# Kernel optimization log

Measured on AMD Instinct MI355X. Metric: run time of the kernel, lower is better.

The kernel has to match this reference:

```python
import jax, jax.numpy as jnp
import numpy as np

N = 100000      # nodes
E = 1600000     # edges (avg degree 16)
D_IN = 128      # in_channels
D_OUT = 64      # out_channels (heads=1)
SCALE_PARAM = 2.0


def setup_inputs() -> dict:
    key = jax.random.key(0)
    ks = jax.random.split(key, 10)
    x = jax.random.normal(ks[0], (N, D_IN), dtype=jnp.float32)
    edge_index = jax.random.randint(ks[1], (2, E), 0, N, dtype=jnp.int64)
    s = 0.05
    Wq = jax.random.normal(ks[2], (D_IN, D_OUT), dtype=jnp.float32) * s
    bq = jax.random.normal(ks[3], (D_OUT,), dtype=jnp.float32) * s
    Wk = jax.random.normal(ks[4], (D_IN, D_OUT), dtype=jnp.float32) * s
    bk = jax.random.normal(ks[5], (D_OUT,), dtype=jnp.float32) * s
    Wv = jax.random.normal(ks[6], (D_IN, D_OUT), dtype=jnp.float32) * s
    bv = jax.random.normal(ks[7], (D_OUT,), dtype=jnp.float32) * s
    Wskip = jax.random.normal(ks[8], (D_IN, D_OUT), dtype=jnp.float32) * s
    bskip = jax.random.normal(ks[9], (D_OUT,), dtype=jnp.float32) * s
    return {"x": x, "edge_index": edge_index, "Wq": Wq, "bq": bq,
            "Wk": Wk, "bk": bk, "Wv": Wv, "bv": bv,
            "Wskip": Wskip, "bskip": bskip}


def reference(x, edge_index, Wq, bq, Wk, bk, Wv, bv, Wskip, bskip):
    # TransformerConvReducrLayer forward (heads=1, no edge_attr, eval mode)
    q = x @ Wq + bq          # [N, C]
    k = x @ Wk + bk          # [N, C]
    v = x @ Wv + bv          # [N, C]
    src = edge_index[0]      # source node j
    dst = edge_index[1]      # target node i
    inv_sqrt_c = np.float32(1.0 / np.sqrt(D_OUT))
    # per-edge attention logits: (query_i * key_j).sum(-1) / sqrt(C)
    alpha = jnp.sum(q[dst] * k[src], axis=-1) * inv_sqrt_c  # [E]
    # custom non-softmax normalization (global mean/std, torch unbiased std)
    alpha = alpha - jnp.mean(alpha)
    alpha = alpha / ((1.0 / np.float32(SCALE_PARAM)) * jnp.std(alpha, ddof=1))
    alpha = jax.nn.sigmoid(alpha)
    # message = value_j * alpha, scatter-add to target nodes
    msg = v[src] * alpha[:, None]                           # [E, C]
    out = jnp.zeros((N, D_OUT), dtype=x.dtype).at[dst].add(msg)
    # root/skip connection (TransformerConv root_weight=True, beta=False)
    out = out + x @ Wskip + bskip
    return out
```

## Files before the change

### kernel.cpp

```cpp
#include <hip/hip_runtime.h>
#include <math.h>

#define D_IN 128
#define D_OUT 64
#define SCALE_PARAM 2.0f
#define NSLOT 64
#define SLOT_STRIDE 16
#define NPB_LOG 9
#define NPB 512
#define MAXBUCK 256
#define MS_NBLK 256

typedef unsigned short ushortt;
typedef __attribute__((ext_vector_type(8))) short bf16x8;
typedef __attribute__((ext_vector_type(4))) float f32x4;

__device__ __forceinline__ ushortt f2bf(float f) {
    union { float f; unsigned u; } cv; cv.f = f;
    unsigned u = cv.u;
    return (ushortt)((u + 0x7FFFu + ((u >> 16) & 1u)) >> 16);
}
__device__ __forceinline__ unsigned cvt_pk_bf16(float a, float b) {
    unsigned r;
    asm("v_cvt_pk_bf16_f32 %0, %1, %2" : "=v"(r) : "v"(a), "v"(b));
    return r;
}
__device__ __forceinline__ float dot2bf(unsigned a, unsigned b, float c) {
    float d;
    asm("v_dot2_f32_bf16 %0, %1, %2, %3" : "=v"(d) : "v"(a), "v"(b), "v"(c));
    return d;
}
__device__ __forceinline__ float bflo(unsigned w) {
    union { unsigned u; float f; } cv; cv.u = w << 16;
    return cv.f;
}
__device__ __forceinline__ float bfhi(unsigned w) {
    union { unsigned u; float f; } cv; cv.u = w & 0xFFFF0000u;
    return cv.f;
}

__global__ __launch_bounds__(256) void prep_w_kernel(
    const float* __restrict__ Wq, const float* __restrict__ Wk,
    const float* __restrict__ Wv, const float* __restrict__ Ws,
    uint4* __restrict__ wfrag)
{
    const int gid = blockIdx.x * 256 + threadIdx.x;
    const int l  = gid & 63;
    const int ci = (gid >> 6) & 3;
    const int ks = (gid >> 8) & 3;
    const int m  = (gid >> 10) & 3;
    const float* Wm = (m == 0) ? Wq : (m == 1) ? Wk : (m == 2) ? Wv : Ws;
    const int cl = l & 15;
    const int kb8 = (l >> 4) * 8;
    unsigned pk[4];
#pragma unroll
    for (int p = 0; p < 4; ++p) {
        float f0 = Wm[(ks * 32 + kb8 + 2 * p)     * D_OUT + ci * 16 + cl];
        float f1 = Wm[(ks * 32 + kb8 + 2 * p + 1) * D_OUT + ci * 16 + cl];
        pk[p] = (unsigned)f2bf(f0) | ((unsigned)f2bf(f1) << 16);
    }
    wfrag[gid] = make_uint4(pk[0], pk[1], pk[2], pk[3]);
}

__global__ __launch_bounds__(256) void fused_gemm_kernel(
    const float* __restrict__ x, const uint4* __restrict__ wfrag,
    const float* __restrict__ bq, const float* __restrict__ bk,
    const float* __restrict__ bv, const float* __restrict__ bs,
    ushortt* __restrict__ q, ushortt* __restrict__ kk, ushortt* __restrict__ v,
    float* __restrict__ skip, int N)
{
    __shared__ __align__(16) ushortt As[64 * 128];
    char* AsB = (char*)As;

    const int t = threadIdx.x;
    const int w = t >> 6;
    const int l = t & 63;
    const int cl = l & 15;
    const int kb8 = (l >> 4) * 8;
    const int rbase = (l >> 4) * 4;
    const int row0 = blockIdx.x * 64;

    const float* bp = (w == 0) ? bq : (w == 1) ? bk : (w == 2) ? bv : bs;

    float4 xv[8];
#pragma unroll
    for (int i = 0; i < 8; ++i) {
        int f = i * 256 + t;
        int r = f >> 5;
        int k4 = f & 31;
        int grow = row0 + r;
        xv[i] = make_float4(0.f, 0.f, 0.f, 0.f);
        if (grow < N)
            xv[i] = *reinterpret_cast<const float4*>(&x[(size_t)grow * D_IN + k4 * 4]);
    }

    union U8 { uint4 u; bf16x8 v; };
    bf16x8 bfr[4][4];
#pragma unroll
    for (int ks = 0; ks < 4; ++ks)
#pragma unroll
        for (int ci = 0; ci < 4; ++ci) {
            U8 tmp; tmp.u = wfrag[((w * 4 + ks) * 4 + ci) * 64 + l];
            bfr[ks][ci] = tmp.v;
        }
    float4 bias4[4];
#pragma unroll
    for (int ci = 0; ci < 4; ++ci)
        bias4[ci] = reinterpret_cast<const float4*>(bp)[ci * 4 + (l >> 4)];

#pragma unroll
    for (int i = 0; i < 8; ++i) {
        int f = i * 256 + t;
        int r = f >> 5;
        int k4 = f & 31;
        uint2 pk;
        pk.x = cvt_pk_bf16(xv[i].x, xv[i].y);
        pk.y = cvt_pk_bf16(xv[i].z, xv[i].w);
        int addr = r * 256 + ((k4 * 8) ^ ((r & 7) << 4));
        *reinterpret_cast<uint2*>(AsB + addr) = pk;
    }
    __syncthreads();

    f32x4 acc[4][4];
#pragma unroll
    for (int ri = 0; ri < 4; ++ri)
#pragma unroll
        for (int ci = 0; ci < 4; ++ci) acc[ri][ci] = (f32x4)(0.f);

#pragma unroll
    for (int ks = 0; ks < 4; ++ks) {
        bf16x8 afr[4];
#pragma unroll
        for (int ri = 0; ri < 4; ++ri) {
            int row = ri * 16 + cl;
            int kby = ks * 64 + kb8 * 2;
            int addr = row * 256 + (kby ^ ((row & 7) << 4));
            afr[ri] = *reinterpret_cast<const bf16x8*>(AsB + addr);
        }
#pragma unroll
        for (int ri = 0; ri < 4; ++ri)
#pragma unroll
            for (int ci = 0; ci < 4; ++ci)
                acc[ri][ci] = __builtin_amdgcn_mfma_f32_16x16x32_bf16(
                    bfr[ks][ci], afr[ri], acc[ri][ci], 0, 0, 0);
    }

    ushortt* qkv = (w == 0) ? q : (w == 1) ? kk : v;
#pragma unroll
    for (int ri = 0; ri < 4; ++ri) {
        int grow = row0 + ri * 16 + cl;
        if (grow >= N) continue;
        if (w == 3) {
#pragma unroll
            for (int ci = 0; ci < 4; ++ci) {
                float4 o;
                o.x = acc[ri][ci][0] + bias4[ci].x;
                o.y = acc[ri][ci][1] + bias4[ci].y;
                o.z = acc[ri][ci][2] + bias4[ci].z;
                o.w = acc[ri][ci][3] + bias4[ci].w;
                *reinterpret_cast<float4*>(&skip[(size_t)grow * D_OUT + ci * 16 + rbase]) = o;
            }
        } else {
#pragma unroll
            for (int ci = 0; ci < 4; ++ci) {
                uint2 pk;
                pk.x = cvt_pk_bf16(acc[ri][ci][0] + bias4[ci].x,
                                   acc[ri][ci][1] + bias4[ci].y);
                pk.y = cvt_pk_bf16(acc[ri][ci][2] + bias4[ci].z,
                                   acc[ri][ci][3] + bias4[ci].w);
                *reinterpret_cast<uint2*>(&qkv[(size_t)grow * D_OUT + ci * 16 + rbase]) = pk;
            }
        }
    }
}

__global__ __launch_bounds__(256) void coarse_hist_kernel(
    const int* __restrict__ dst, int* __restrict__ ccnt, int E)
{
    __shared__ int lc[MAXBUCK];
    const int t = threadIdx.x;
    if (t < MAXBUCK) lc[t] = 0;
    __syncthreads();
    const int stride = gridDim.x * 256 * 4;
    for (int base = (blockIdx.x * 256 + t) * 4; base < E; base += stride) {
        if (base + 3 < E) {
            int4 d = *reinterpret_cast<const int4*>(&dst[base]);
            atomicAdd(&lc[d.x >> NPB_LOG], 1);
            atomicAdd(&lc[d.y >> NPB_LOG], 1);
            atomicAdd(&lc[d.z >> NPB_LOG], 1);
            atomicAdd(&lc[d.w >> NPB_LOG], 1);
        } else {
            for (int i = base; i < E; ++i) atomicAdd(&lc[dst[i] >> NPB_LOG], 1);
        }
    }
    __syncthreads();
    if (t < MAXBUCK && lc[t]) atomicAdd(&ccnt[t], lc[t]);
}

__global__ void coarse_scan_kernel(const int* __restrict__ ccnt,
                                   int* __restrict__ bb, int* __restrict__ tails,
                                   int NBUCK)
{
    if (threadIdx.x == 0) {
        int run = 0;
        for (int b = 0; b < NBUCK; ++b) {
            bb[b] = run;
            tails[b] = run;
            run += ccnt[b];
        }
        bb[NBUCK] = run;
    }
}

__global__ __launch_bounds__(1024) void multisplit_kernel(
    const int* __restrict__ src, const int* __restrict__ dst,
    int* __restrict__ tails, unsigned* __restrict__ ebuf, int E)
{
    __shared__ int cnt[MAXBUCK];
    __shared__ int cur[MAXBUCK];
    __shared__ int base_l[MAXBUCK];
    const int t = threadIdx.x;
    const int blk = blockIdx.x;
    const int e0 = (int)((long long)blk * E / MS_NBLK);
    const int e1 = (int)((long long)(blk + 1) * E / MS_NBLK);
    if (t < MAXBUCK) { cnt[t] = 0; cur[t] = 0; }
    __syncthreads();
    for (int e = e0 + t; e < e1; e += 1024)
        atomicAdd(&cnt[dst[e] >> NPB_LOG], 1);
    __syncthreads();
    if (t < MAXBUCK) {
        int c = cnt[t];
        base_l[t] = c ? atomicAdd(&tails[t], c) : 0;
    }
    __syncthreads();
    for (int e = e0 + t; e < e1; e += 1024) {
        int d = dst[e];
        int b = d >> NPB_LOG;
        int r = atomicAdd(&cur[b], 1);
        ebuf[base_l[b] + r] = ((unsigned)(d & (NPB - 1)) << 17) | (unsigned)src[e];
    }
}

__global__ __launch_bounds__(512) void fine_sort_kernel(
    const unsigned* __restrict__ ebuf, const int* __restrict__ bb,
    int* __restrict__ sorted_src, int* __restrict__ row_start,
    int N, int NBUCK)
{
    __shared__ int cnt[NPB];
    __shared__ int cur[NPB];
    __shared__ int wsum[8];
    const int t = threadIdx.x;
    const int b = blockIdx.x;
    const int nbase = b << NPB_LOG;
    const int seg0 = bb[b], seg1 = bb[b + 1];

    cnt[t] = 0; cur[t] = 0;
    __syncthreads();
    for (int j = seg0 + t; j < seg1; j += 512)
        atomicAdd(&cnt[ebuf[j] >> 17], 1);
    __syncthreads();

    {
        const int lane = t & 63, wid = t >> 6;
        int c = cnt[t];
        int x = c;
#pragma unroll
        for (int off = 1; off < 64; off <<= 1) {
            int n = __shfl_up(x, off, 64);
            if (lane >= off) x += n;
        }
        if (lane == 63) wsum[wid] = x;
        __syncthreads();
        int woff = 0;
        for (int w = 0; w < wid; ++w) woff += wsum[w];
        int excl = x - c + woff;
        cnt[t] = excl;
        int node = nbase + t;
        if (node < N) row_start[node] = seg0 + excl;
    }
    if (b == NBUCK - 1 && t == 0) row_start[N] = seg1;
    __syncthreads();

    for (int j = seg0 + t; j < seg1; j += 512) {
        unsigned u = ebuf[j];
        int dl = u >> 17;
        int r = atomicAdd(&cur[dl], 1);
        sorted_src[seg0 + cnt[dl] + r] = (int)(u & 0x1FFFFu);
    }
}

__global__ __launch_bounds__(256) void node_logit_kernel(
    const ushortt* __restrict__ q, const ushortt* __restrict__ k,
    const int* __restrict__ sorted_src, const int* __restrict__ row_start,
    float* __restrict__ alpha_sorted, float* __restrict__ slots, int N)
{
    const int t = threadIdx.x;
    const int wid = t >> 6, lane = t & 63;
    const int g = lane >> 3;
    const int c8 = lane & 7;
    const int node = blockIdx.x * 4 + wid;
    float lsum = 0.f, lsq = 0.f;
    if (node < N) {
        const uint4 qw = reinterpret_cast<const uint4*>(q + (size_t)node * D_OUT)[c8];
        const int s0 = row_start[node], s1 = row_start[node + 1];
        for (int j0 = s0; j0 < s1; j0 += 32) {
            const int nb = min(s1 - j0, 32);
            int sv = 0;
            if (lane < nb) sv = sorted_src[j0 + lane];
            uint4 kw[4];
#pragma unroll
            for (int it = 0; it < 4; ++it) {
                int sidx = __shfl(sv, it * 8 + g, 64);
                kw[it] = make_uint4(0u, 0u, 0u, 0u);
                if (it * 8 + g < nb)
                    kw[it] = reinterpret_cast<const uint4*>(k + (size_t)sidx * D_OUT)[c8];
            }
#pragma unroll
            for (int it = 0; it < 4; ++it) {
                const bool valid = it * 8 + g < nb;
                float p = dot2bf(qw.x, kw[it].x, 0.f);
                p = dot2bf(qw.y, kw[it].y, p);
                p = dot2bf(qw.z, kw[it].z, p);
                p = dot2bf(qw.w, kw[it].w, p);
                p += __shfl_xor(p, 1, 8);
                p += __shfl_xor(p, 2, 8);
                p += __shfl_xor(p, 4, 8);
                if (valid && c8 == 0) {
                    float a = p * 0.125f;
                    alpha_sorted[j0 + it * 8 + g] = a;
                    lsum += a;
                    lsq += a * a;
                }
            }
        }
    }
#pragma unroll
    for (int off = 1; off < 64; off <<= 1) {
        lsum += __shfl_xor(lsum, off, 64);
        lsq  += __shfl_xor(lsq,  off, 64);
    }
    __shared__ float red[2][4];
    if (lane == 0) { red[0][wid] = lsum; red[1][wid] = lsq; }
    __syncthreads();
    if (t == 0) {
        float* sl = slots + (blockIdx.x & (NSLOT - 1)) * SLOT_STRIDE;
        atomicAdd(&sl[0], red[0][0] + red[0][1] + red[0][2] + red[0][3]);
        atomicAdd(&sl[1], red[1][0] + red[1][1] + red[1][2] + red[1][3]);
    }
}

__global__ void finalize_stats_kernel(const float* __restrict__ slots,
                                      float* stats, int E) {
    const int lane = threadIdx.x & 63;
    float s  = slots[lane * SLOT_STRIDE];
    float s2 = slots[lane * SLOT_STRIDE + 1];
#pragma unroll
    for (int off = 1; off < 64; off <<= 1) {
        s  += __shfl_xor(s,  off, 64);
        s2 += __shfl_xor(s2, off, 64);
    }
    if (lane == 0) {
        float mean = s / (float)E;
        float var = (s2 - (float)E * mean * mean) / (float)(E - 1);
        stats[2] = mean;
        stats[3] = SCALE_PARAM / sqrtf(var);
    }
}

__global__ __launch_bounds__(256) void node_gather_kernel(
    const ushortt* __restrict__ v, const int* __restrict__ sorted_src,
    const float* __restrict__ alpha_sorted, const int* __restrict__ row_start,
    const float* __restrict__ stats, float* __restrict__ out, int N)
{
    const int t = threadIdx.x;
    const int wid = t >> 6, lane = t & 63;
    const int g = lane >> 3, c8 = lane & 7;
    const int node = blockIdx.x * 4 + wid;
    if (node >= N) return;
    const float mean = stats[2], coef = stats[3];
    float a0 = 0, a1 = 0, a2 = 0, a3 = 0, a4 = 0, a5 = 0, a6 = 0, a7 = 0;
    const int s0 = row_start[node], s1 = row_start[node + 1];
    for (int j0 = s0; j0 < s1; j0 += 32) {
        const int nb = min(s1 - j0, 32);
        int sv = 0;
        float av = 0.f;
        if (lane < nb) {
            sv = sorted_src[j0 + lane];
            float al = alpha_sorted[j0 + lane];
            al = (al - mean) * coef;
            av = 1.f / (1.f + __expf(-al));
        }
        uint4 vw[4];
        float alv[4];
#pragma unroll
        for (int it = 0; it < 4; ++it) {
            int sidx = __shfl(sv, it * 8 + g, 64);
            alv[it] = __shfl(av, it * 8 + g, 64);
            vw[it] = make_uint4(0u, 0u, 0u, 0u);
            if (it * 8 + g < nb)
                vw[it] = reinterpret_cast<const uint4*>(v + (size_t)sidx * D_OUT)[c8];
        }
#pragma unroll
        for (int it = 0; it < 4; ++it) {
            const float al = (it * 8 + g < nb) ? alv[it] : 0.f;
            a0 = fmaf(bflo(vw[it].x), al, a0); a1 = fmaf(bfhi(vw[it].x), al, a1);
            a2 = fmaf(bflo(vw[it].y), al, a2); a3 = fmaf(bfhi(vw[it].y), al, a3);
            a4 = fmaf(bflo(vw[it].z), al, a4); a5 = fmaf(bfhi(vw[it].z), al, a5);
            a6 = fmaf(bflo(vw[it].w), al, a6); a7 = fmaf(bfhi(vw[it].w), al, a7);
        }
    }
#pragma unroll
    for (int off = 8; off < 64; off <<= 1) {
        a0 += __shfl_xor(a0, off, 64); a1 += __shfl_xor(a1, off, 64);
        a2 += __shfl_xor(a2, off, 64); a3 += __shfl_xor(a3, off, 64);
        a4 += __shfl_xor(a4, off, 64); a5 += __shfl_xor(a5, off, 64);
        a6 += __shfl_xor(a6, off, 64); a7 += __shfl_xor(a7, off, 64);
    }
    if (g == 0) {
        float* op = out + (size_t)node * D_OUT + c8 * 8;
        float4 c0 = *reinterpret_cast<float4*>(op);
        float4 c1 = *reinterpret_cast<float4*>(op + 4);
        c0.x += a0; c0.y += a1; c0.z += a2; c0.w += a3;
        c1.x += a4; c1.y += a5; c1.z += a6; c1.w += a7;
        *reinterpret_cast<float4*>(op)     = c0;
        *reinterpret_cast<float4*>(op + 4) = c1;
    }
}

extern "C" void kernel_launch(void* const* d_in, const int* in_sizes, int n_in,
                              void* d_out, int out_size, void* d_ws, size_t ws_size,
                              hipStream_t stream) {
    const float* x     = (const float*)d_in[0];
    const int*   eidx  = (const int*)d_in[1];
    const float* Wq    = (const float*)d_in[2];
    const float* bq    = (const float*)d_in[3];
    const float* Wk    = (const float*)d_in[4];
    const float* bk    = (const float*)d_in[5];
    const float* Wv    = (const float*)d_in[6];
    const float* bv    = (const float*)d_in[7];
    const float* Ws    = (const float*)d_in[8];
    const float* bs    = (const float*)d_in[9];
    float* out = (float*)d_out;

    const int N = in_sizes[0] / D_IN;
    const int E = in_sizes[1] / 2;
    const int* src = eidx;
    const int* dst = eidx + E;
    const int NBUCK = (N + NPB - 1) >> NPB_LOG;

    char* base = (char*)d_ws;
    size_t cur = 0;
    auto carve = [&](size_t bytes) -> char* {
        char* p = base + cur;
        cur = (cur + bytes + 255) & ~(size_t)255;
        return p;
    };
    const size_t nodebf = (size_t)N * D_OUT * sizeof(ushortt);
    ushortt* q          = (ushortt*)carve(nodebf);
    ushortt* k          = (ushortt*)carve(nodebf);
    ushortt* v          = (ushortt*)carve(nodebf);
    float* alpha_sorted = (float*)carve((size_t)E * sizeof(float));
    int*   sorted_src   = (int*)carve((size_t)E * sizeof(int));
    unsigned* ebuf      = (unsigned*)carve((size_t)E * sizeof(unsigned));
    uint4* wfrag        = (uint4*)carve(4096 * sizeof(uint4));
    const size_t ccnt_b  = (MAXBUCK * sizeof(int) + 255) & ~(size_t)255;
    const size_t slots_b = (size_t)NSLOT * SLOT_STRIDE * sizeof(float);
    char*  zreg         = carve(ccnt_b + slots_b + 256);
    int*   ccnt         = (int*)zreg;
    float* slots        = (float*)(zreg + ccnt_b);
    float* stats        = (float*)(zreg + ccnt_b + slots_b);
    int*   row_start    = (int*)carve((size_t)(N + 1) * sizeof(int));
    int*   bb           = (int*)carve((size_t)(MAXBUCK + 1) * sizeof(int));
    int*   tails        = (int*)carve((size_t)MAXBUCK * sizeof(int));

    hipMemsetAsync(zreg, 0, ccnt_b + slots_b + 256, stream);

    prep_w_kernel<<<16, 256, 0, stream>>>(Wq, Wk, Wv, Ws, wfrag);

    coarse_hist_kernel<<<512, 256, 0, stream>>>(dst, ccnt, E);
    coarse_scan_kernel<<<1, 64, 0, stream>>>(ccnt, bb, tails, NBUCK);
    multisplit_kernel<<<MS_NBLK, 1024, 0, stream>>>(src, dst, tails, ebuf, E);

    const int gemm_grid = (N + 63) / 64;
    fused_gemm_kernel<<<gemm_grid, 256, 0, stream>>>(
        x, wfrag, bq, bk, bv, bs, q, k, v, out, N);

    fine_sort_kernel<<<NBUCK, 512, 0, stream>>>(
        ebuf, bb, sorted_src, row_start, N, NBUCK);

    node_logit_kernel<<<(N + 3) / 4, 256, 0, stream>>>(
        q, k, sorted_src, row_start, alpha_sorted, slots, N);
    finalize_stats_kernel<<<1, 64, 0, stream>>>(slots, stats, E);
    node_gather_kernel<<<(N + 3) / 4, 256, 0, stream>>>(
        v, sorted_src, alpha_sorted, row_start, stats, out, N);
}
```

Before: 176.8 us.

## Fuse weight prep with histogram and multisplit with GEMM via block-range dispatch

Merges the weight-fragment prep kernel with the coarse destination histogram into one launch. The multisplit (edge bucketing) kernel is merged into the node GEMM kernel, with the first 512 blocks doing multisplit at 256 threads and the rest doing GEMM rows. The aim is to cut launch count and let the memory-bound edge scatter overlap with the GEMM instead of running serially. Multisplit now uses smaller blocks, twice as many of them, and shared memory reused from the GEMM tile buffer. This may change the per-block atomic contention on the global tails.

```diff
diff --git a/kernel.cpp b/kernel.cpp
--- a/kernel.cpp
+++ b/kernel.cpp
@@ -9,7 +9,8 @@
 #define NPB_LOG 9
 #define NPB 512
 #define MAXBUCK 256
-#define MS_NBLK 256
+#define MSF_NBLK 512
+#define PREP_BLKS 16
 
 typedef unsigned short ushortt;
 typedef __attribute__((ext_vector_type(8))) short bf16x8;
@@ -39,46 +40,114 @@
     return cv.f;
 }
 
-__global__ __launch_bounds__(256) void prep_w_kernel(
+__global__ __launch_bounds__(256) void prep_hist_kernel(
     const float* __restrict__ Wq, const float* __restrict__ Wk,
     const float* __restrict__ Wv, const float* __restrict__ Ws,
-    uint4* __restrict__ wfrag)
-{
-    const int gid = blockIdx.x * 256 + threadIdx.x;
-    const int l  = gid & 63;
-    const int ci = (gid >> 6) & 3;
-    const int ks = (gid >> 8) & 3;
-    const int m  = (gid >> 10) & 3;
-    const float* Wm = (m == 0) ? Wq : (m == 1) ? Wk : (m == 2) ? Wv : Ws;
-    const int cl = l & 15;
-    const int kb8 = (l >> 4) * 8;
-    unsigned pk[4];
-#pragma unroll
-    for (int p = 0; p < 4; ++p) {
-        float f0 = Wm[(ks * 32 + kb8 + 2 * p)     * D_OUT + ci * 16 + cl];
-        float f1 = Wm[(ks * 32 + kb8 + 2 * p + 1) * D_OUT + ci * 16 + cl];
-        pk[p] = (unsigned)f2bf(f0) | ((unsigned)f2bf(f1) << 16);
-    }
-    wfrag[gid] = make_uint4(pk[0], pk[1], pk[2], pk[3]);
-}
-
-__global__ __launch_bounds__(256) void fused_gemm_kernel(
+    uint4* __restrict__ wfrag,
+    const int* __restrict__ dst, int* __restrict__ ccnt, int E)
+{
+    __shared__ int lc[MAXBUCK];
+    const int t = threadIdx.x;
+    if (blockIdx.x < PREP_BLKS) {
+        const int gid = blockIdx.x * 256 + t;
+        const int l  = gid & 63;
+        const int ci = (gid >> 6) & 3;
+        const int ks = (gid >> 8) & 3;
+        const int m  = (gid >> 10) & 3;
+        const float* Wm = (m == 0) ? Wq : (m == 1) ? Wk : (m == 2) ? Wv : Ws;
+        const int cl = l & 15;
+        const int kb8 = (l >> 4) * 8;
+        unsigned pk[4];
+#pragma unroll
+        for (int p = 0; p < 4; ++p) {
+            float f0 = Wm[(ks * 32 + kb8 + 2 * p)     * D_OUT + ci * 16 + cl];
+            float f1 = Wm[(ks * 32 + kb8 + 2 * p + 1) * D_OUT + ci * 16 + cl];
+            pk[p] = (unsigned)f2bf(f0) | ((unsigned)f2bf(f1) << 16);
+        }
+        wfrag[gid] = make_uint4(pk[0], pk[1], pk[2], pk[3]);
+    } else {
+        const int blk = blockIdx.x - PREP_BLKS;
+        const int nblk = gridDim.x - PREP_BLKS;
+        if (t < MAXBUCK) lc[t] = 0;
+        __syncthreads();
+        const int stride = nblk * 256 * 4;
+        for (int base = (blk * 256 + t) * 4; base < E; base += stride) {
+            if (base + 3 < E) {
+                int4 d = *reinterpret_cast<const int4*>(&dst[base]);
+                atomicAdd(&lc[d.x >> NPB_LOG], 1);
+                atomicAdd(&lc[d.y >> NPB_LOG], 1);
+                atomicAdd(&lc[d.z >> NPB_LOG], 1);
+                atomicAdd(&lc[d.w >> NPB_LOG], 1);
+            } else {
+                for (int i = base; i < E; ++i) atomicAdd(&lc[dst[i] >> NPB_LOG], 1);
+            }
+        }
+        __syncthreads();
+        if (t < MAXBUCK && lc[t]) atomicAdd(&ccnt[t], lc[t]);
+    }
+}
+
+__global__ void coarse_scan_kernel(const int* __restrict__ ccnt,
+                                   int* __restrict__ bb, int* __restrict__ tails,
+                                   int NBUCK)
+{
+    if (threadIdx.x == 0) {
+        int run = 0;
+        for (int b = 0; b < NBUCK; ++b) {
+            bb[b] = run;
+            tails[b] = run;
+            run += ccnt[b];
+        }
+        bb[NBUCK] = run;
+    }
+}
+
+__global__ __launch_bounds__(256) void gemm_ms_kernel(
     const float* __restrict__ x, const uint4* __restrict__ wfrag,
     const float* __restrict__ bq, const float* __restrict__ bk,
     const float* __restrict__ bv, const float* __restrict__ bs,
     ushortt* __restrict__ q, ushortt* __restrict__ kk, ushortt* __restrict__ v,
-    float* __restrict__ skip, int N)
-{
-    __shared__ __align__(16) ushortt As[64 * 128];
-    char* AsB = (char*)As;
-
+    float* __restrict__ skip, int N,
+    const int* __restrict__ src, const int* __restrict__ dst,
+    int* __restrict__ tails, unsigned* __restrict__ ebuf, int E)
+{
+    __shared__ __align__(16) char smem[64 * 128 * 2];
     const int t = threadIdx.x;
+
+    if (blockIdx.x < MSF_NBLK) {
+        int* cnt    = (int*)smem;
+        int* curc   = (int*)(smem + 1024);
+        int* base_l = (int*)(smem + 2048);
+        const int blk = blockIdx.x;
+        const int e0 = (int)((long long)blk * E / MSF_NBLK);
+        const int e1 = (int)((long long)(blk + 1) * E / MSF_NBLK);
+        if (t < MAXBUCK) { cnt[t] = 0; curc[t] = 0; }
+        __syncthreads();
+        for (int e = e0 + t; e < e1; e += 256)
+            atomicAdd(&cnt[dst[e] >> NPB_LOG], 1);
+        __syncthreads();
+        if (t < MAXBUCK) {
+            int c = cnt[t];
+            base_l[t] = c ? atomicAdd(&tails[t], c) : 0;
+        }
+        __syncthreads();
+        for (int e = e0 + t; e < e1; e += 256) {
+            int d = dst[e];
+            int b = d >> NPB_LOG;
+            int r = atomicAdd(&curc[b], 1);
+            ebuf[base_l[b] + r] = ((unsigned)(d & (NPB - 1)) << 17) | (unsigned)src[e];
+        }
+        return;
+    }
+
+    ushortt* As = (ushortt*)smem;
+    char* AsB = smem;
     const int w = t >> 6;
     const int l = t & 63;
     const int cl = l & 15;
     const int kb8 = (l >> 4) * 8;
     const int rbase = (l >> 4) * 4;
-    const int row0 = blockIdx.x * 64;
+    const int row0 = (blockIdx.x - MSF_NBLK) * 64;
 
     const float* bp = (w == 0) ? bq : (w == 1) ? bk : (w == 2) ? bv : bs;
 
@@ -171,73 +240,6 @@
                 *reinterpret_cast<uint2*>(&qkv[(size_t)grow * D_OUT + ci * 16 + rbase]) = pk;
             }
         }
-    }
-}
-
-__global__ __launch_bounds__(256) void coarse_hist_kernel(
-    const int* __restrict__ dst, int* __restrict__ ccnt, int E)
-{
-    __shared__ int lc[MAXBUCK];
-    const int t = threadIdx.x;
-    if (t < MAXBUCK) lc[t] = 0;
-    __syncthreads();
-    const int stride = gridDim.x * 256 * 4;
-    for (int base = (blockIdx.x * 256 + t) * 4; base < E; base += stride) {
-        if (base + 3 < E) {
-            int4 d = *reinterpret_cast<const int4*>(&dst[base]);
-            atomicAdd(&lc[d.x >> NPB_LOG], 1);
-            atomicAdd(&lc[d.y >> NPB_LOG], 1);
-            atomicAdd(&lc[d.z >> NPB_LOG], 1);
-            atomicAdd(&lc[d.w >> NPB_LOG], 1);
-        } else {
-            for (int i = base; i < E; ++i) atomicAdd(&lc[dst[i] >> NPB_LOG], 1);
-        }
-    }
-    __syncthreads();
-    if (t < MAXBUCK && lc[t]) atomicAdd(&ccnt[t], lc[t]);
-}
-
-__global__ void coarse_scan_kernel(const int* __restrict__ ccnt,
-                                   int* __restrict__ bb, int* __restrict__ tails,
-                                   int NBUCK)
-{
-    if (threadIdx.x == 0) {
-        int run = 0;
-        for (int b = 0; b < NBUCK; ++b) {
-            bb[b] = run;
-            tails[b] = run;
-            run += ccnt[b];
-        }
-        bb[NBUCK] = run;
-    }
-}
-
-__global__ __launch_bounds__(1024) void multisplit_kernel(
-    const int* __restrict__ src, const int* __restrict__ dst,
-    int* __restrict__ tails, unsigned* __restrict__ ebuf, int E)
-{
-    __shared__ int cnt[MAXBUCK];
-    __shared__ int cur[MAXBUCK];
-    __shared__ int base_l[MAXBUCK];
-    const int t = threadIdx.x;
-    const int blk = blockIdx.x;
-    const int e0 = (int)((long long)blk * E / MS_NBLK);
-    const int e1 = (int)((long long)(blk + 1) * E / MS_NBLK);
-    if (t < MAXBUCK) { cnt[t] = 0; cur[t] = 0; }
-    __syncthreads();
-    for (int e = e0 + t; e < e1; e += 1024)
-        atomicAdd(&cnt[dst[e] >> NPB_LOG], 1);
-    __syncthreads();
-    if (t < MAXBUCK) {
-        int c = cnt[t];
-        base_l[t] = c ? atomicAdd(&tails[t], c) : 0;
-    }
-    __syncthreads();
-    for (int e = e0 + t; e < e1; e += 1024) {
-        int d = dst[e];
-        int b = d >> NPB_LOG;
-        int r = atomicAdd(&cur[b], 1);
-        ebuf[base_l[b] + r] = ((unsigned)(d & (NPB - 1)) << 17) | (unsigned)src[e];
     }
 }
 
@@ -475,15 +477,14 @@
 
     hipMemsetAsync(zreg, 0, ccnt_b + slots_b + 256, stream);
 
-    prep_w_kernel<<<16, 256, 0, stream>>>(Wq, Wk, Wv, Ws, wfrag);
-
-    coarse_hist_kernel<<<512, 256, 0, stream>>>(dst, ccnt, E);
+    prep_hist_kernel<<<PREP_BLKS + 512, 256, 0, stream>>>(
+        Wq, Wk, Wv, Ws, wfrag, dst, ccnt, E);
     coarse_scan_kernel<<<1, 64, 0, stream>>>(ccnt, bb, tails, NBUCK);
-    multisplit_kernel<<<MS_NBLK, 1024, 0, stream>>>(src, dst, tails, ebuf, E);
 
     const int gemm_grid = (N + 63) / 64;
-    fused_gemm_kernel<<<gemm_grid, 256, 0, stream>>>(
-        x, wfrag, bq, bk, bv, bs, q, k, v, out, N);
+    gemm_ms_kernel<<<MSF_NBLK + gemm_grid, 256, 0, stream>>>(
+        x, wfrag, bq, bk, bv, bs, q, k, v, out, N,
+        src, dst, tails, ebuf, E);
 
     fine_sort_kernel<<<NBUCK, 512, 0, stream>>>(
         ebuf, bb, sorted_src, row_start, N, NBUCK);
```

Result: no change. 175.6 us (-0.7%).
